# Optimization experiments

Hardware: AMD Instinct MI355X
Metric: run time of the kernel (lower is better)

Reference implementation:

```python
import jax, jax.numpy as jnp
import numpy as np

NUM_MEM, MEM_DIM, INP_DIM, N = 4096, 512, 1024, 32768

def setup_inputs() -> dict:
    key = jax.random.key(0)
    ks = jax.random.split(key, 6)
    s = 1.0 / np.sqrt(MEM_DIM)
    return {
        "k": jax.random.normal(ks[0], (N, INP_DIM), dtype=jnp.float32),
        "mem": jax.random.normal(ks[1], (NUM_MEM, MEM_DIM), dtype=jnp.float32),
        "fk_w": jax.random.uniform(ks[2], (INP_DIM, MEM_DIM), jnp.float32, -s, s),
        "fk_b": jax.random.uniform(ks[3], (INP_DIM,), jnp.float32, -s, s),
        "fv_w": jax.random.uniform(ks[4], (INP_DIM, MEM_DIM), jnp.float32, -s, s),
        "fv_b": jax.random.uniform(ks[5], (INP_DIM,), jnp.float32, -s, s),
    }

def reference(k, mem, fk_w, fk_b, fv_w, fv_b):
    # key/value derivation from the memory bank: [num_mem, inp_dim]
    key = jax.nn.softmax(mem @ fk_w.T + fk_b, axis=-1)
    val = jax.nn.relu(mem @ fv_w.T + fv_b)
    # attention read: [n, num_mem]
    att = jax.nn.softmax(k @ key.T, axis=-1)
    # output: [n, inp_dim]
    return att @ val
```

## Files before the change

### kernel.cpp

```cpp
#include <hip/hip_runtime.h>
#include <stdint.h>

typedef unsigned short u16;
typedef short s16x8 __attribute__((ext_vector_type(8)));
typedef float f32x4 __attribute__((ext_vector_type(4)));

__device__ __forceinline__ u16 f2bf(float f) {
    union { float f; uint32_t i; } v; v.f = f;
    return (u16)((v.i + 0x7FFFu + ((v.i >> 16) & 1u)) >> 16);
}

__global__ void __launch_bounds__(256) cvt_f32_bf16(
    const float* __restrict__ src, u16* __restrict__ dst, int n4)
{
    int i = blockIdx.x * 256 + threadIdx.x;
    if (i >= n4) return;
    float4 f = ((const float4*)src)[i];
    ushort4 o;
    o.x = f2bf(f.x); o.y = f2bf(f.y); o.z = f2bf(f.z); o.w = f2bf(f.w);
    ((ushort4*)dst)[i] = o;
}

#define ASYNC_LD16(gp, lp)                                                       \
    __builtin_amdgcn_global_load_lds(                                            \
        (const __attribute__((address_space(1))) uint32_t*)(gp),                 \
        (__attribute__((address_space(3))) uint32_t*)(lp), 16, 0, 0)

template <int MODE>
__global__ void __launch_bounds__(256) gemm_bt(
    const u16* __restrict__ A, const u16* __restrict__ B, int K, int N,
    u16* __restrict__ C, float* __restrict__ Cf,
    const float* __restrict__ bias,
    const float* __restrict__ sv, float* __restrict__ sum_out)
{
    __shared__ __align__(16) u16 As[128 * 32];
    __shared__ __align__(16) u16 Bs[128 * 32];

    const int tid  = threadIdx.x;
    const int lane = tid & 63;
    const int wave = tid >> 6;
    const int wx = wave & 1, wy = wave >> 1;
    const int lr = lane & 15, lq = lane >> 4;
    const int m0 = blockIdx.y * 128, n0 = blockIdx.x * 128;

    f32x4 acc[4][4] = {};

    const int srow = tid >> 2;
    const int scol = (tid & 3) * 8;
    const u16* gA = A + (size_t)(m0 + srow) * K + scol;
    const u16* gB = B + (size_t)(n0 + srow) * K + scol;
    const size_t rstep = (size_t)64 * K;
    u16* lA0 = &As[wave * 512];
    u16* lA1 = &As[2048 + wave * 512];
    u16* lB0 = &Bs[wave * 512];
    u16* lB1 = &Bs[2048 + wave * 512];

    const u16* pa = &As[(wy * 64 + lr) * 32 + lq * 8];
    const u16* pb = &Bs[(wx * 64 + lr) * 32 + lq * 8];

    for (int k0 = 0; k0 < K; k0 += 32) {
        ASYNC_LD16(gA + k0, lA0);
        ASYNC_LD16(gA + k0 + rstep, lA1);
        ASYNC_LD16(gB + k0, lB0);
        ASYNC_LD16(gB + k0 + rstep, lB1);
        __syncthreads();
        s16x8 af[4], bfr[4];
#pragma unroll
        for (int i = 0; i < 4; ++i) {
            af[i]  = *(const s16x8*)(pa + i * 512);
            bfr[i] = *(const s16x8*)(pb + i * 512);
        }
#pragma unroll
        for (int mi = 0; mi < 4; ++mi)
#pragma unroll
            for (int ni = 0; ni < 4; ++ni)
                acc[mi][ni] = __builtin_amdgcn_mfma_f32_16x16x32_bf16(
                    af[mi], bfr[ni], acc[mi][ni], 0, 0, 0);
        __syncthreads();
    }

    const int rowB = m0 + wy * 64 + lq * 4;
    const int colB = n0 + wx * 64 + lr;

    if constexpr (MODE == 0) {
        float bcol[4];
#pragma unroll
        for (int ni = 0; ni < 4; ++ni) bcol[ni] = bias[colB + ni * 16];
#pragma unroll
        for (int mi = 0; mi < 4; ++mi)
#pragma unroll
            for (int r = 0; r < 4; ++r) {
                const int gm = rowB + mi * 16 + r;
                float s = 0.f;
#pragma unroll
                for (int ni = 0; ni < 4; ++ni) {
                    float e = __expf(acc[mi][ni][r] + bcol[ni]);
                    C[(size_t)gm * N + (colB + ni * 16)] = f2bf(e);
                    s += e;
                }
                s += __shfl_xor(s, 1);
                s += __shfl_xor(s, 2);
                s += __shfl_xor(s, 4);
                s += __shfl_xor(s, 8);
                if (lr == 0) atomicAdd(&sum_out[gm], s);
            }
    } else if constexpr (MODE == 1) {
#pragma unroll
        for (int mi = 0; mi < 4; ++mi)
#pragma unroll
            for (int r = 0; r < 4; ++r) {
                const int gm = rowB + mi * 16 + r;
                const float b = bias[gm];
#pragma unroll
                for (int ni = 0; ni < 4; ++ni) {
                    float c = acc[mi][ni][r] + b;
                    C[(size_t)gm * N + (colB + ni * 16)] = f2bf(c > 0.f ? c : 0.f);
                }
            }
    } else if constexpr (MODE == 2) {
        float inv[4];
#pragma unroll
        for (int ni = 0; ni < 4; ++ni) inv[ni] = 1.0f / sv[colB + ni * 16];
#pragma unroll
        for (int mi = 0; mi < 4; ++mi)
#pragma unroll
            for (int r = 0; r < 4; ++r) {
                const int gm = rowB + mi * 16 + r;
                float s = 0.f;
#pragma unroll
                for (int ni = 0; ni < 4; ++ni) {
                    float e = __expf(acc[mi][ni][r] * inv[ni]);
                    C[(size_t)gm * N + (colB + ni * 16)] = f2bf(e);
                    s += e;
                }
                s += __shfl_xor(s, 1);
                s += __shfl_xor(s, 2);
                s += __shfl_xor(s, 4);
                s += __shfl_xor(s, 8);
                if (lr == 0) atomicAdd(&sum_out[gm], s);
            }
    } else {
#pragma unroll
        for (int mi = 0; mi < 4; ++mi)
#pragma unroll
            for (int r = 0; r < 4; ++r) {
                const int gm = rowB + mi * 16 + r;
                const float invr = 1.0f / sv[gm];
#pragma unroll
                for (int ni = 0; ni < 4; ++ni)
                    Cf[(size_t)gm * N + (colB + ni * 16)] = acc[mi][ni][r] * invr;
            }
    }
}

extern "C" void kernel_launch(void* const* d_in, const int* in_sizes, int n_in,
                              void* d_out, int out_size, void* d_ws, size_t ws_size,
                              hipStream_t stream)
{
    (void)in_sizes; (void)n_in; (void)out_size;
    const float* kin = (const float*)d_in[0];
    const float* mem = (const float*)d_in[1];
    const float* fkw = (const float*)d_in[2];
    const float* fkb = (const float*)d_in[3];
    const float* fvw = (const float*)d_in[4];
    const float* fvb = (const float*)d_in[5];
    float* out = (float*)d_out;

    const int NM = 4096, MD = 512, ID = 1024, NQ = 32768;

    u16* kbf   = (u16*)d_ws;
    u16* membf = kbf   + (size_t)NQ * ID;
    u16* fkwbf = membf + (size_t)NM * MD;
    u16* fvwbf = fkwbf + (size_t)ID * MD;
    u16* expK  = fvwbf + (size_t)ID * MD;
    u16* valT  = expK  + (size_t)NM * ID;
    u16* P     = valT  + (size_t)ID * NM;
    float* rsK = (float*)(P + (size_t)NQ * NM);
    float* rs2 = rsK + NM;
    const size_t needed = (size_t)((char*)(rs2 + NQ) - (char*)d_ws);
    if (ws_size < needed) return;

    hipMemsetAsync(rsK, 0, (size_t)(NM + NQ) * sizeof(float), stream);

    cvt_f32_bf16<<<(NQ * ID / 4 + 255) / 256, 256, 0, stream>>>(kin, kbf, NQ * ID / 4);
    cvt_f32_bf16<<<(NM * MD / 4 + 255) / 256, 256, 0, stream>>>(mem, membf, NM * MD / 4);
    cvt_f32_bf16<<<(ID * MD / 4 + 255) / 256, 256, 0, stream>>>(fkw, fkwbf, ID * MD / 4);
    cvt_f32_bf16<<<(ID * MD / 4 + 255) / 256, 256, 0, stream>>>(fvw, fvwbf, ID * MD / 4);

    gemm_bt<0><<<dim3(ID / 128, NM / 128), 256, 0, stream>>>(
        membf, fkwbf, MD, ID, expK, nullptr, fkb, nullptr, rsK);
    gemm_bt<1><<<dim3(NM / 128, ID / 128), 256, 0, stream>>>(
        fvwbf, membf, MD, NM, valT, nullptr, fvb, nullptr, nullptr);
    gemm_bt<2><<<dim3(NM / 128, NQ / 128), 256, 0, stream>>>(
        kbf, expK, ID, NM, P, nullptr, nullptr, rsK, rs2);
    gemm_bt<3><<<dim3(ID / 128, NQ / 128), 256, 0, stream>>>(
        P, valT, NM, ID, nullptr, out, nullptr, rs2, nullptr);
}
```

Before: 1.129 ms.

## Use 256x256 multi-buffered pipelined GEMM for the two large attention matmuls

Adds a new 512-thread GEMM kernel with 256x256 tiles, a 4-stage async global-to-LDS buffer ring, an XOR-swizzled LDS layout, grid swizzling for L2 locality, and s_setprio around the MFMA blocks. The two large GEMMs (scores with exp, and the final normalized output) move to it. The aim is to remove the per-iteration load-then-sync stall of the old single-buffered 128x128 kernel and raise data reuse per tile. In exchange it uses 128KB of LDS and many more accumulator registers, which limits occupancy.

```diff
diff --git a/kernel.cpp b/kernel.cpp
--- a/kernel.cpp
+++ b/kernel.cpp
@@ -104,7 +104,7 @@
                 s += __shfl_xor(s, 8);
                 if (lr == 0) atomicAdd(&sum_out[gm], s);
             }
-    } else if constexpr (MODE == 1) {
+    } else {
 #pragma unroll
         for (int mi = 0; mi < 4; ++mi)
 #pragma unroll
@@ -117,12 +117,106 @@
                     C[(size_t)gm * N + (colB + ni * 16)] = f2bf(c > 0.f ? c : 0.f);
                 }
             }
-    } else if constexpr (MODE == 2) {
+    }
+}
+
+template <int MODE>
+__global__ void __launch_bounds__(512, 2) gemm256_bt(
+    const u16* __restrict__ A, const u16* __restrict__ B, int K, int N,
+    u16* __restrict__ C, float* __restrict__ Cf,
+    const float* __restrict__ sv, float* __restrict__ sum_out, int nbx)
+{
+    __shared__ __align__(16) u16 lds[4 * 16384];
+
+    const int tid  = threadIdx.x;
+    const int lane = tid & 63;
+    const int wave = tid >> 6;
+    const int wr = wave >> 2;
+    const int wc = wave & 3;
+    const int fr = lane & 15;
+    const int lq = lane >> 4;
+
+    const int nwg = gridDim.x;
+    const int swz = ((int)blockIdx.x & 7) * (nwg >> 3) + ((int)blockIdx.x >> 3);
+    const int bx = swz % nbx, by = swz / nbx;
+    const int m0 = by * 256, n0 = bx * 256;
+
+    const int r0 = tid >> 2;
+    const int r1 = r0 + 128;
+    const int gch = (tid & 3) ^ ((r0 >> 1) & 3);
+    const u16* gA0 = A + (size_t)(m0 + r0) * K + gch * 8;
+    const u16* gA1 = A + (size_t)(m0 + r1) * K + gch * 8;
+    const u16* gB0 = B + (size_t)(n0 + r0) * K + gch * 8;
+    const u16* gB1 = B + (size_t)(n0 + r1) * K + gch * 8;
+
+#define STG_A(bf_, kt_) do {                                                  \
+        ASYNC_LD16(gA0 + (kt_) * 32, lds + (bf_) * 16384 + wave * 512);       \
+        ASYNC_LD16(gA1 + (kt_) * 32, lds + (bf_) * 16384 + 4096 + wave * 512);\
+    } while (0)
+#define STG_B(bf_, kt_) do {                                                  \
+        ASYNC_LD16(gB0 + (kt_) * 32, lds + (bf_) * 16384 + 8192 + wave * 512);\
+        ASYNC_LD16(gB1 + (kt_) * 32, lds + (bf_) * 16384 + 12288 + wave * 512);\
+    } while (0)
+
+    const int rch = lq ^ ((fr >> 1) & 3);
+    const int offA0 = (wr * 128 + fr) * 32 + rch * 8;
+    const int offB0 = (wc * 64 + fr) * 32 + rch * 8;
+
+    f32x4 acc[8][4] = {};
+    const int NT = K >> 5;
+
+    STG_A(0, 0); STG_B(0, 0);
+    STG_A(1, 1); STG_B(1, 1);
+    STG_A(2, 2); STG_B(2, 2);
+    asm volatile("s_waitcnt vmcnt(8)" ::: "memory");
+    __builtin_amdgcn_s_barrier();
+
+    for (int c = 0; c < NT; ++c) {
+        const u16* sA = lds + (c & 3) * 16384;
+        const u16* sB = sA + 8192;
+        s16x8 a0[4], b0[4], a1[4];
+#pragma unroll
+        for (int i = 0; i < 4; ++i) a0[i] = *(const s16x8*)(sA + offA0 + i * 512);
+#pragma unroll
+        for (int i = 0; i < 4; ++i) b0[i] = *(const s16x8*)(sB + offB0 + i * 512);
+        if (c + 3 < NT) STG_A((c + 3) & 3, c + 3);
+        __builtin_amdgcn_s_barrier();
+        asm volatile("s_waitcnt lgkmcnt(0)" ::: "memory");
+        __builtin_amdgcn_s_setprio(1);
+#pragma unroll
+        for (int mi = 0; mi < 4; ++mi)
+#pragma unroll
+            for (int ni = 0; ni < 4; ++ni)
+                acc[mi][ni] = __builtin_amdgcn_mfma_f32_16x16x32_bf16(
+                    a0[mi], b0[ni], acc[mi][ni], 0, 0, 0);
+        __builtin_amdgcn_s_setprio(0);
+        __builtin_amdgcn_s_barrier();
+#pragma unroll
+        for (int i = 0; i < 4; ++i) a1[i] = *(const s16x8*)(sA + offA0 + (i + 4) * 512);
+        if (c + 3 < NT) STG_B((c + 3) & 3, c + 3);
+        __builtin_amdgcn_s_barrier();
+        asm volatile("s_waitcnt lgkmcnt(0)" ::: "memory");
+        __builtin_amdgcn_s_setprio(1);
+#pragma unroll
+        for (int mi = 0; mi < 4; ++mi)
+#pragma unroll
+            for (int ni = 0; ni < 4; ++ni)
+                acc[mi + 4][ni] = __builtin_amdgcn_mfma_f32_16x16x32_bf16(
+                    a1[mi], b0[ni], acc[mi + 4][ni], 0, 0, 0);
+        __builtin_amdgcn_s_setprio(0);
+        asm volatile("s_waitcnt vmcnt(8)" ::: "memory");
+        __builtin_amdgcn_s_barrier();
+    }
+
+    const int rowB = m0 + wr * 128 + lq * 4;
+    const int colB = n0 + wc * 64 + fr;
+
+    if constexpr (MODE == 2) {
         float inv[4];
 #pragma unroll
         for (int ni = 0; ni < 4; ++ni) inv[ni] = 1.0f / sv[colB + ni * 16];
 #pragma unroll
-        for (int mi = 0; mi < 4; ++mi)
+        for (int mi = 0; mi < 8; ++mi)
 #pragma unroll
             for (int r = 0; r < 4; ++r) {
                 const int gm = rowB + mi * 16 + r;
@@ -137,11 +231,11 @@
                 s += __shfl_xor(s, 2);
                 s += __shfl_xor(s, 4);
                 s += __shfl_xor(s, 8);
-                if (lr == 0) atomicAdd(&sum_out[gm], s);
+                if (fr == 0) atomicAdd(&sum_out[gm], s);
             }
     } else {
 #pragma unroll
-        for (int mi = 0; mi < 4; ++mi)
+        for (int mi = 0; mi < 8; ++mi)
 #pragma unroll
             for (int r = 0; r < 4; ++r) {
                 const int gm = rowB + mi * 16 + r;
@@ -151,6 +245,8 @@
                     Cf[(size_t)gm * N + (colB + ni * 16)] = acc[mi][ni][r] * invr;
             }
     }
+#undef STG_A
+#undef STG_B
 }
 
 extern "C" void kernel_launch(void* const* d_in, const int* in_sizes, int n_in,
@@ -191,8 +287,8 @@
         membf, fkwbf, MD, ID, expK, nullptr, fkb, nullptr, rsK);
     gemm_bt<1><<<dim3(NM / 128, ID / 128), 256, 0, stream>>>(
         fvwbf, membf, MD, NM, valT, nullptr, fvb, nullptr, nullptr);
-    gemm_bt<2><<<dim3(NM / 128, NQ / 128), 256, 0, stream>>>(
-        kbf, expK, ID, NM, P, nullptr, nullptr, rsK, rs2);
-    gemm_bt<3><<<dim3(ID / 128, NQ / 128), 256, 0, stream>>>(
-        P, valT, NM, ID, nullptr, out, nullptr, rs2, nullptr);
-}
+    gemm256_bt<2><<<(NQ / 256) * (NM / 256), 512, 0, stream>>>(
+        kbf, expK, ID, NM, P, nullptr, rsK, rs2, NM / 256);
+    gemm256_bt<3><<<(NQ / 256) * (ID / 256), 512, 0, stream>>>(
+        P, valT, NM, ID, nullptr, out, rs2, nullptr, ID / 256);
+}
```

Result: faster. 921.6 us (-18.3%).
